# Kernel optimization log

Measured on AMD Instinct MI355X. Metric: run time of the kernel, lower is better.

## Reference

```python
import jax, jax.numpy as jnp
import numpy as np

T, H, WD = 30, 41, 2048            # timesteps, freq rows, time frames
N_SEC, SEC_LEN, IN_SEC = 9, 4, 6   # conv sections, section stride, input section size
KH, KW = 6, 40                     # conv kernel
FM = 50                            # feature maps
THRESH = 23.0                      # fire threshold
POOL = 4                           # pooling kernel/stride
SEC_H = IN_SEC + SEC_LEN - 1       # 9 rows fed to each section conv


def setup_inputs() -> dict:
    key = jax.random.key(0)
    k1, k2 = jax.random.split(key)
    x = jax.random.uniform(k1, (T, 1, H, WD), dtype=jnp.float32)
    W = jax.random.normal(k2, (N_SEC, FM, 1, KH, KW), dtype=jnp.float32)
    return {"x": x, "W": W}


def _conv_section(sec, w):
    # sec: (T,1,SEC_H,WD) treated as batch of T images; w: (FM,1,KH,KW)
    return jax.lax.conv_general_dilated(
        sec, w, window_strides=(1, 1), padding="VALID",
        dimension_numbers=("NCHW", "OIHW", "NCHW"))


def _forward(x, W):
    # slice 9 overlapping frequency sections: rows i*4 .. i*4+9
    secs = jnp.stack([
        jax.lax.dynamic_slice_in_dim(x, i * SEC_LEN, SEC_H, axis=2)
        for i in range(N_SEC)
    ])  # (9, T, 1, 9, WD)
    pots = jax.vmap(_conv_section)(secs, W)          # (9, T, FM, 4, WD-KW+1)
    spks = (pots > THRESH).astype(pots.dtype)        # sf.fire(threshold=23)
    # snn.Pooling((4,4)) == max_pool2d kernel=stride=(4,4)
    pooled = jax.lax.reduce_window(
        spks, -jnp.inf, jax.lax.max,
        (1, 1, 1, POOL, POOL), (1, 1, 1, POOL, POOL), "VALID")  # (9,T,FM,1,Wp)
    # ties broken by potential at first-spike time; winners[0][0] = feature map.
    has = pooled > 0
    any_spk = has.any(axis=1)                        # (9, FM, 1, Wp)
    t_first = jnp.argmax(has, axis=1)                # (9, FM, 1, Wp)
    pot_at = jnp.take_along_axis(pooled, t_first[:, None], axis=1)[:, 0]
    BIG = jnp.float32(T * 1000.0)
    score = jnp.where(any_spk,
                      (T - t_first).astype(pooled.dtype) * BIG + pot_at,
                      -jnp.inf)                      # (9, FM, 1, Wp)
    flat = score.reshape(N_SEC, -1)
    idx = jnp.argmax(flat, axis=1)
    spatial = score.shape[-1] * score.shape[-2]
    feat = idx // spatial                            # winner feature map per section
    feat = jnp.where(jnp.isneginf(flat.max(axis=1)), -1, feat)  # output=-1 if no winner
    return pooled, feat


def reference(x, W):
    return _forward(x, W)
```

## Files before the change

### kernel.cpp

```cpp
#include <hip/hip_runtime.h>

#define T_ 30
#define H_ 41
#define WD_ 2048
#define NSEC 9
#define FM 50
#define WP 502
#define THRESH 23.0f
#define POOLED_SIZE (NSEC * T_ * FM * WP)
#define MARGIN 0.125f
#define NFRAG 18432

typedef _Float16 half8 __attribute__((ext_vector_type(8)));
typedef _Float16 half4v __attribute__((ext_vector_type(4)));
typedef float f32x4 __attribute__((ext_vector_type(4)));

__device__ __forceinline__ unsigned short f16_bits(float f) {
    union { _Float16 h; unsigned short s; } u;
    u.h = (_Float16)f;
    return u.s;
}

__global__ __launch_bounds__(256) void prep_kernel(
    const float* __restrict__ Wg, int* __restrict__ wsi,
    uint4* __restrict__ wfh)
{
    const int gid = blockIdx.x * 256 + threadIdx.x;
    if (gid < NSEC) wsi[gid] = 0x7fffffff;
    if (gid >= NFRAG) return;
    const int blk = gid & 31;
    const int fm  = (gid >> 5) & 63;
    const int sec = gid >> 11;
    const int t0  = blk * 8;
    const bool valid = (t0 < 240) && (fm < FM);
    const float* wp = Wg + ((size_t)sec * FM + (valid ? fm : 0)) * 240 + (valid ? t0 : 0);
    float4 wa = *reinterpret_cast<const float4*>(wp);
    float4 wb = *reinterpret_cast<const float4*>(wp + 4);
    float f[8] = {wa.x, wa.y, wa.z, wa.w, wb.x, wb.y, wb.z, wb.w};
    unsigned hh[4];
#pragma unroll
    for (int i = 0; i < 4; ++i) {
        unsigned h0 = f16_bits(valid ? f[2 * i] : 0.f);
        unsigned h1 = f16_bits(valid ? f[2 * i + 1] : 0.f);
        hh[i] = (h1 << 16) | h0;
    }
    wfh[gid] = *reinterpret_cast<uint4*>(hh);
}

template <bool PRE>
__global__ __launch_bounds__(256) void conv_pool_kernel(
    const float* __restrict__ x, const float* __restrict__ Wg,
    const uint4* __restrict__ wfh,
    float* __restrict__ out, int* __restrict__ keys)
{
    __shared__ __align__(16) unsigned short xh[4][10][192];
    __shared__ int sred[256];

    const int b       = blockIdx.x;
    const int coltile = b & 15;
    const int tt      = (b >> 4) % T_;
    const int sec     = b / 480;
    const int w0      = coltile * 128;
    const int rowbase = 4 * sec;
    const int tid     = threadIdx.x;

    for (int i = tid; i < 440; i += 256) {
        const int row = i / 44;
        const int c4  = i % 44;
        const int grow = (rowbase + row < H_) ? rowbase + row : H_ - 1;
        const int gc   = w0 + 4 * c4;
        float4 v;
        if (gc + 3 < WD_) {
            v = *reinterpret_cast<const float4*>(x + ((size_t)tt * H_ + grow) * WD_ + gc);
        } else {
            v.x = v.y = v.z = v.w = 0.f;
        }
        float f[4] = {v.x, v.y, v.z, v.w};
        unsigned short hq[4];
#pragma unroll
        for (int e = 0; e < 4; ++e) hq[e] = f16_bits(f[e]);
        const int xr = (row & 7) << 3;
#pragma unroll
        for (int S = 0; S < 4; ++S)
#pragma unroll
            for (int e = 0; e < 4; ++e) {
                const int j = 4 * c4 + e - S;
                if (j >= 0 && j < 176) xh[S][row][j ^ xr] = hq[e];
            }
    }
    __syncthreads();

    const int L    = tid & 63;
    const int j_p  = tid >> 6;
    const int q    = L >> 4;
    const int n16  = L & 15;

    int pA[8], pB[8];
#pragma unroll
    for (int kk = 0; kk < 8; ++kk) {
        const int t0 = 32 * kk + 8 * q;
        const int r  = t0 / 40;
        const int c0 = t0 - 40 * r;
        const int row = j_p + r;
        const int xr  = (row & 7) << 3;
        const int s   = c0 + 8 * n16;
        pA[kk] = row * 192 + (s ^ xr);
        pB[kk] = row * 192 + ((s + 8) ^ xr);
    }

    unsigned long long cmask[4];
#pragma unroll
    for (int reg = 0; reg < 4; ++reg)
        cmask[reg] = __ballot(w0 + 8 * (q * 4 + reg) <= 2000);

    unsigned mask = 0;

#pragma unroll 1
    for (int ft = 0; ft < 4; ++ft) {
        const int fm = ft * 16 + n16;
        const unsigned long long fmmask = __ballot(fm < FM);
        half8 wh[8];
        if (PRE) {
            const int fb = (sec * 64 + ft * 16 + n16) * 32 + q;
#pragma unroll
            for (int kk = 0; kk < 8; ++kk) {
                union { uint4 u; half8 h; } c1;
                c1.u = wfh[fb + 4 * kk];
                wh[kk] = c1.h;
            }
        } else {
#pragma unroll
            for (int kk = 0; kk < 8; ++kk) {
                const int t0 = 32 * kk + 8 * q;
                const bool wvalid = (t0 < 240) && (fm < FM);
                const float* wp = Wg + (size_t)sec * FM * 240 +
                                  (size_t)(wvalid ? fm : 0) * 240 + (wvalid ? t0 : 0);
                float4 wa = *reinterpret_cast<const float4*>(wp);
                float4 wb = *reinterpret_cast<const float4*>(wp + 4);
                float f[8] = {wa.x, wa.y, wa.z, wa.w, wb.x, wb.y, wb.z, wb.w};
                union { unsigned u[4]; half8 h; } c1;
#pragma unroll
                for (int i = 0; i < 4; ++i) {
                    unsigned h0 = f16_bits(wvalid ? f[2 * i] : 0.f);
                    unsigned h1 = f16_bits(wvalid ? f[2 * i + 1] : 0.f);
                    c1.u[i] = (h1 << 16) | h0;
                }
                wh[kk] = c1.h;
            }
        }

#pragma unroll 1
        for (int S = 0; S < 4; ++S) {
            const unsigned short* hb = &xh[S][0][0];

            f32x4 acc0 = {0.f, 0.f, 0.f, 0.f};
            f32x4 acc1 = {0.f, 0.f, 0.f, 0.f};
#pragma unroll
            for (int kk = 0; kk < 8; ++kk) {
                half8 ah0 = *reinterpret_cast<const half8*>(hb + pA[kk]);
                half4v h1 = *reinterpret_cast<const half4v*>(hb + pB[kk]);
                half8 hx  = __builtin_shufflevector(h1, h1, 0, 1, 2, 3, 0, 1, 2, 3);
                half8 ah1 = __builtin_shufflevector(ah0, hx, 4, 5, 6, 7, 8, 9, 10, 11);
                acc0 = __builtin_amdgcn_mfma_f32_16x16x32_f16(ah0, wh[kk], acc0, 0, 0, 0);
                acc1 = __builtin_amdgcn_mfma_f32_16x16x32_f16(ah1, wh[kk], acc1, 0, 0, 0);
            }

            auto epilogue = [&](const f32x4& acc, const int res) {
#pragma unroll
                for (int reg = 0; reg < 4; ++reg) {
                    const float a = acc[reg];
                    const unsigned bitv = 1u << (reg * 8 + ft * 2 + (res >> 2));
                    const bool bhi = (a >= THRESH + MARGIN);
                    if (bhi) mask |= bitv;
                    unsigned long long bm =
                        __ballot(a > THRESH - MARGIN) & ~__ballot(bhi) &
                        fmmask & cmask[reg];
                    while (bm) {
                        const int src = __ffsll((long long)bm) - 1;
                        bm &= bm - 1;
                        const int q_s   = src >> 4;
                        const int fm_s  = ft * 16 + (src & 15);
                        const int pcg_s = w0 + res + 8 * (q_s * 4 + reg);
                        float part = 0.f;
#pragma unroll
                        for (int k2 = 0; k2 < 4; ++k2) {
                            const int t = L + 64 * k2;
                            if (t < 240) {
                                const int r2 = t / 40, c2 = t - 40 * r2;
                                part = fmaf(
                                    x[((size_t)tt * H_ + rowbase + j_p + r2) * WD_ + pcg_s + c2],
                                    Wg[(size_t)sec * FM * 240 + (size_t)fm_s * 240 + t],
                                    part);
                            }
                        }
#pragma unroll
                        for (int off = 32; off; off >>= 1)
                            part += __shfl_xor(part, off);
                        if (L == src && part > THRESH)
                            mask |= bitv;
                    }
                }
            };
            epilogue(acc0, S);
            epilogue(acc1, S + 4);
        }
    }

    unsigned* lmask = reinterpret_cast<unsigned*>(sred);
    lmask[j_p * 64 + L] = mask;
    __syncthreads();

    int mykey = 0x7fffffff;
    for (int e = tid; e < 2048; e += 256) {
        const int fmo = e >> 5, p = e & 31;
        const int m = p >> 1, rg = p & 1, ftc = fmo >> 4, fn = fmo & 15;
        const int lane = (m >> 2) * 16 + fn;
        const int bitpos = (m & 3) * 8 + ftc * 2 + rg;
        const unsigned bits = lmask[0 * 64 + lane] | lmask[1 * 64 + lane] |
                              lmask[2 * 64 + lane] | lmask[3 * 64 + lane];
        const int pg = coltile * 32 + p;
        const int spk = (bits >> bitpos) & 1u;
        if (fmo < FM && pg < WP) {
            out[((size_t)(sec * T_ + tt) * FM + fmo) * WP + pg] = spk ? 1.0f : 0.0f;
            if (spk) mykey = min(mykey, fmo * WP + pg);
        }
    }
    __syncthreads();
    sred[tid] = mykey;
    __syncthreads();
    for (int s = 128; s > 0; s >>= 1) {
        if (tid < s) sred[tid] = min(sred[tid], sred[tid + s]);
        __syncthreads();
    }
    if (tid == 0 && sred[0] != 0x7fffffff)
        atomicMin(&keys[sec], (tt << 15) | sred[0]);
}

__global__ void init_kernel(int* __restrict__ ws)
{
    if (threadIdx.x < NSEC) ws[threadIdx.x] = 0x7fffffff;
}

__global__ void finalize_kernel(const int* __restrict__ ws, float* __restrict__ out)
{
    const int i = threadIdx.x;
    if (i < NSEC) {
        const int key = ws[i];
        float feat;
        if (key == 0x7fffffff) feat = -1.0f;
        else                   feat = (float)((key & 32767) / WP);
        out[POOLED_SIZE + i] = feat;
    }
}

extern "C" void kernel_launch(void* const* d_in, const int* in_sizes, int n_in,
                              void* d_out, int out_size, void* d_ws, size_t ws_size,
                              hipStream_t stream) {
    const float* x  = (const float*)d_in[0];
    const float* Wg = (const float*)d_in[1];
    float* out = (float*)d_out;
    int*   wsi = (int*)d_ws;
    uint4* wfh = (uint4*)((char*)d_ws + 256);

    const bool pre = ws_size >= 256 + (size_t)NFRAG * 16;
    if (pre) {
        prep_kernel<<<dim3(72), dim3(256), 0, stream>>>(Wg, wsi, wfh);
        conv_pool_kernel<true><<<dim3(4320), dim3(256), 0, stream>>>(x, Wg, wfh, out, wsi);
    } else {
        init_kernel<<<dim3(1), dim3(64), 0, stream>>>(wsi);
        conv_pool_kernel<false><<<dim3(4320), dim3(256), 0, stream>>>(x, Wg, wfh, out, wsi);
    }
    finalize_kernel<<<dim3(1), dim3(16), 0, stream>>>(wsi, out);
}
```

Measured before the change: 167.0 us.

## Merge two adjacent column tiles into one 512-thread block sharing the input halo

Each block now covers 256 output columns with 8 waves (two halves of 4 waves) in place of 128 columns with 4 waves. The shared fp16 input staging tile is widened to 304 columns, so the 40-column convolution halo is loaded and converted once per pair of tiles rather than twice. The grid is halved and the mask and min reductions grow to 512 threads. The trade is larger shared memory per block, bigger barriers and fewer blocks, which may affect occupancy and scheduling.

```diff
diff --git a/kernel.cpp b/kernel.cpp
--- a/kernel.cpp
+++ b/kernel.cpp
@@ -10,6 +10,7 @@
 #define POOLED_SIZE (NSEC * T_ * FM * WP)
 #define MARGIN 0.125f
 #define NFRAG 18432
+#define RS 384
 
 typedef _Float16 half8 __attribute__((ext_vector_type(8)));
 typedef _Float16 half4v __attribute__((ext_vector_type(4)));
@@ -48,27 +49,27 @@
 }
 
 template <bool PRE>
-__global__ __launch_bounds__(256) void conv_pool_kernel(
+__global__ __launch_bounds__(512, 8) void conv_pool_kernel(
     const float* __restrict__ x, const float* __restrict__ Wg,
     const uint4* __restrict__ wfh,
     float* __restrict__ out, int* __restrict__ keys)
 {
-    __shared__ __align__(16) unsigned short xh[4][10][192];
-    __shared__ int sred[256];
+    __shared__ __align__(16) unsigned short xh[4][10][RS];
+    __shared__ int sred[512];
 
     const int b       = blockIdx.x;
-    const int coltile = b & 15;
-    const int tt      = (b >> 4) % T_;
-    const int sec     = b / 480;
-    const int w0      = coltile * 128;
+    const int pair    = b & 7;
+    const int tt      = (b >> 3) % T_;
+    const int sec     = b / 240;
+    const int w0A     = pair * 256;
     const int rowbase = 4 * sec;
     const int tid     = threadIdx.x;
 
-    for (int i = tid; i < 440; i += 256) {
-        const int row = i / 44;
-        const int c4  = i % 44;
+    for (int i = tid; i < 760; i += 512) {
+        const int row = i / 76;
+        const int c4  = i % 76;
         const int grow = (rowbase + row < H_) ? rowbase + row : H_ - 1;
-        const int gc   = w0 + 4 * c4;
+        const int gc   = w0A + 4 * c4;
         float4 v;
         if (gc + 3 < WD_) {
             v = *reinterpret_cast<const float4*>(x + ((size_t)tt * H_ + grow) * WD_ + gc);
@@ -85,15 +86,18 @@
 #pragma unroll
             for (int e = 0; e < 4; ++e) {
                 const int j = 4 * c4 + e - S;
-                if (j >= 0 && j < 176) xh[S][row][j ^ xr] = hq[e];
+                if (j >= 0 && j < 304) xh[S][row][j ^ xr] = hq[e];
             }
     }
     __syncthreads();
 
     const int L    = tid & 63;
-    const int j_p  = tid >> 6;
+    const int wid  = tid >> 6;
+    const int half = wid >> 2;
+    const int j_p  = wid & 3;
     const int q    = L >> 4;
     const int n16  = L & 15;
+    const int w0   = w0A + half * 128;
 
     int pA[8], pB[8];
 #pragma unroll
@@ -103,9 +107,9 @@
         const int c0 = t0 - 40 * r;
         const int row = j_p + r;
         const int xr  = (row & 7) << 3;
-        const int s   = c0 + 8 * n16;
-        pA[kk] = row * 192 + (s ^ xr);
-        pB[kk] = row * 192 + ((s + 8) ^ xr);
+        const int s   = c0 + 8 * n16 + half * 128;
+        pA[kk] = row * RS + (s ^ xr);
+        pB[kk] = row * RS + ((s + 8) ^ xr);
     }
 
     unsigned long long cmask[4];
@@ -207,18 +211,22 @@
     }
 
     unsigned* lmask = reinterpret_cast<unsigned*>(sred);
-    lmask[j_p * 64 + L] = mask;
+    lmask[wid * 64 + L] = mask;
     __syncthreads();
 
     int mykey = 0x7fffffff;
-    for (int e = tid; e < 2048; e += 256) {
-        const int fmo = e >> 5, p = e & 31;
+    for (int e = tid; e < 4096; e += 512) {
+        const int hf  = e >> 11;
+        const int sub = e & 2047;
+        const int fmo = sub >> 5, p = sub & 31;
         const int m = p >> 1, rg = p & 1, ftc = fmo >> 4, fn = fmo & 15;
         const int lane = (m >> 2) * 16 + fn;
         const int bitpos = (m & 3) * 8 + ftc * 2 + rg;
-        const unsigned bits = lmask[0 * 64 + lane] | lmask[1 * 64 + lane] |
-                              lmask[2 * 64 + lane] | lmask[3 * 64 + lane];
-        const int pg = coltile * 32 + p;
+        const unsigned bits = lmask[(hf * 4 + 0) * 64 + lane] |
+                              lmask[(hf * 4 + 1) * 64 + lane] |
+                              lmask[(hf * 4 + 2) * 64 + lane] |
+                              lmask[(hf * 4 + 3) * 64 + lane];
+        const int pg = (pair * 2 + hf) * 32 + p;
         const int spk = (bits >> bitpos) & 1u;
         if (fmo < FM && pg < WP) {
             out[((size_t)(sec * T_ + tt) * FM + fmo) * WP + pg] = spk ? 1.0f : 0.0f;
@@ -228,7 +236,7 @@
     __syncthreads();
     sred[tid] = mykey;
     __syncthreads();
-    for (int s = 128; s > 0; s >>= 1) {
+    for (int s = 256; s > 0; s >>= 1) {
         if (tid < s) sred[tid] = min(sred[tid], sred[tid + s]);
         __syncthreads();
     }
@@ -265,10 +273,10 @@
     const bool pre = ws_size >= 256 + (size_t)NFRAG * 16;
     if (pre) {
         prep_kernel<<<dim3(72), dim3(256), 0, stream>>>(Wg, wsi, wfh);
-        conv_pool_kernel<true><<<dim3(4320), dim3(256), 0, stream>>>(x, Wg, wfh, out, wsi);
+        conv_pool_kernel<true><<<dim3(2160), dim3(512), 0, stream>>>(x, Wg, wfh, out, wsi);
     } else {
         init_kernel<<<dim3(1), dim3(64), 0, stream>>>(wsi);
-        conv_pool_kernel<false><<<dim3(4320), dim3(256), 0, stream>>>(x, Wg, wfh, out, wsi);
+        conv_pool_kernel<false><<<dim3(2160), dim3(512), 0, stream>>>(x, Wg, wfh, out, wsi);
     }
     finalize_kernel<<<dim3(1), dim3(16), 0, stream>>>(wsi, out);
 }
```

Measured after the change: 565.6 us. +238.7%, slower.
